# Kernel optimization log

Hardware: AMD Instinct MI355X
Metric: run time of the kernel (lower is better)

## Reference

```python
import jax, jax.numpy as jnp
import numpy as np


def setup_inputs() -> dict:
    key = jax.random.key(0)
    ks = jax.random.split(key, 7)
    S, B, D = 8, 32768, 512
    k = 1.0 / np.sqrt(D)
    u = lambda kk, shape: jax.random.uniform(kk, shape, jnp.float32, -k, k)
    return {
        "x": jax.random.normal(ks[0], (S, B, D), jnp.float32),
        "weight_ih": u(ks[1], (3 * D, D)),
        "weight_hh": u(ks[2], (3 * D, D)),
        "bias_ih": u(ks[3], (3 * D,)),
        "bias_hh": u(ks[4], (3 * D,)),
        "w1": u(ks[5], (D, D)),
        "w2": u(ks[6], (D, D)),
    }


def _gru_cell(xi, h, weight_ih, weight_hh, bias_ih, bias_hh):
    # PyTorch GRUCell gate order: r, z, n
    gi = xi @ weight_ih.T + bias_ih  # [B, 3H]
    gh = h @ weight_hh.T + bias_hh   # [B, 3H]
    i_r, i_z, i_n = jnp.split(gi, 3, axis=-1)
    h_r, h_z, h_n = jnp.split(gh, 3, axis=-1)
    r = jax.nn.sigmoid(i_r + h_r)
    z = jax.nn.sigmoid(i_z + h_z)
    n = jnp.tanh(i_n + r * h_n)
    return (1.0 - z) * n + z * h


def reference(x, weight_ih, weight_hh, bias_ih, bias_hh, w1, w2):
    S, B, _ = x.shape
    H = w1.shape[0]

    def step(carry, inp):
        h, x_prev = carry
        xi, i = inp
        h = _gru_cell(xi, h, weight_ih, weight_hh, bias_ih, bias_hh)
        mixed = h @ w1.T + x_prev @ w2.T  # uses x[i-1]
        h = jnp.where(i % 2 == 1, mixed, h)
        return (h, xi), None

    h0 = jnp.zeros((B, H), x.dtype)  # hn=None -> zeros
    (hn, _), _ = jax.lax.scan(step, (h0, x[0]), (x, jnp.arange(S)))
    return hn
```

## Files before the change

kernel.cpp:

```cpp
#include <hip/hip_runtime.h>


#define BDIM 32768
#define DDIM 512
#define BD (BDIM * DDIM)

typedef short bf16x8 __attribute__((ext_vector_type(8)));
typedef float f32x4 __attribute__((ext_vector_type(4)));
typedef unsigned short u16x8 __attribute__((ext_vector_type(8)));

#define AS1 __attribute__((address_space(1)))
#define AS3 __attribute__((address_space(3)))

__device__ __forceinline__ unsigned short f2bf(float f) {
  union { float f; unsigned u; } v; v.f = f;
  return (unsigned short)((v.u + 0x7fffu + ((v.u >> 16) & 1u)) >> 16);
}
__device__ __forceinline__ float bf2f(unsigned short b) {
  union { unsigned u; float f; } v; v.u = (unsigned)b << 16; return v.f;
}
__device__ __forceinline__ float sigmf(float x) { return 1.0f / (1.0f + __expf(-x)); }
__device__ __forceinline__ float tanhf_(float x) { return 1.0f - 2.0f / (__expf(2.0f * x) + 1.0f); }
__device__ __forceinline__ void bar() { asm volatile("s_barrier" ::: "memory"); }
#define VMCNT(n) asm volatile("s_waitcnt vmcnt(" #n ")" ::: "memory")

__global__ void cvt_bf16_all(const float* __restrict__ in, unsigned short* __restrict__ out) {
  const size_t stride = (size_t)gridDim.x * 256;
  for (size_t i = (size_t)blockIdx.x * 256 + threadIdx.x; i < (size_t)BD; i += stride) {
    const size_t o = i * 8;
    const float4 a = *(const float4*)(in + o);
    const float4 b = *(const float4*)(in + o + 4);
    u16x8 v;
    v[0] = f2bf(a.x); v[1] = f2bf(a.y); v[2] = f2bf(a.z); v[3] = f2bf(a.w);
    v[4] = f2bf(b.x); v[5] = f2bf(b.y); v[6] = f2bf(b.z); v[7] = f2bf(b.w);
    *(u16x8*)(out + o) = v;
  }
}

__global__ void prep_w(const float* __restrict__ wih, const float* __restrict__ whh,
                       const float* __restrict__ w1, const float* __restrict__ w2,
                       unsigned short* __restrict__ Wg, unsigned short* __restrict__ Wm) {
  int i = blockIdx.x * 256 + threadIdx.x;
  if (i < 1536 * 1024) {
    const int j = i >> 10, k = i & 1023;
    Wg[i] = f2bf((k < 512) ? wih[j * 512 + k] : whh[j * 512 + (k - 512)]);
  } else {
    i -= 1536 * 1024;
    const int j = i >> 10, k = i & 1023;
    Wm[i] = f2bf((k < 512) ? w1[j * 512 + k] : w2[j * 512 + (k - 512)]);
  }
}

__global__ __launch_bounds__(512, 2) void gru_gates(
    const unsigned short* __restrict__ X, const unsigned short* __restrict__ H,
    const unsigned short* __restrict__ Wg, const float* __restrict__ bih,
    const float* __restrict__ bhh, unsigned short* __restrict__ outB) {
  __shared__ char smem[147456];
  const int t = threadIdx.x;
  const int lane = t & 63, wid = t >> 6;
  const int wm = wid >> 1, wn = wid & 1;
  const int xcd = blockIdx.x & 7, ixc = blockIdx.x >> 3;
  const int bm = xcd * 16 + (ixc >> 3);
  const int bn = ixc & 7;

  f32x4 acc[4][8];
  const f32x4 z4 = {0.f, 0.f, 0.f, 0.f};
#pragma unroll
  for (int a = 0; a < 4; ++a)
#pragma unroll
    for (int b = 0; b < 8; ++b) acc[a][b] = z4;

  const int trow = t >> 3;
  const int tswz = ((t & 7) * 16) ^ ((trow & 7) << 4);
  int asrc[4], bsrc[3];
#pragma unroll
  for (int i = 0; i < 4; ++i) asrc[i] = (bm * 256 + i * 64 + trow) * 1024 + tswz;
#pragma unroll
  for (int g = 0; g < 3; ++g) bsrc[g] = (g * 512 + bn * 64 + trow) * 2048 + tswz;

  const char* Xc = (const char*)X;
  const char* Hc = (const char*)H;
  const char* Wc = (const char*)Wg;

  auto issA = [&](int tt, int i) {
    const char* base = ((tt < 8) ? Xc : Hc) + (tt & 7) * 128 + asrc[i];
    __builtin_amdgcn_global_load_lds(
        (const AS1 void*)base,
        (AS3 void*)(smem + (tt % 3) * 32768 + i * 8192 + t * 16), 16, 0, 0);
  };
  auto issB = [&](int tt, int g) {
    const char* base = Wc + tt * 128 + bsrc[g];
    __builtin_amdgcn_global_load_lds(
        (const AS1 void*)base,
        (AS3 void*)(smem + 98304 + (tt & 1) * 24576 + g * 8192 + t * 16), 16, 0, 0);
  };

  issB(0, 0); issB(0, 1); issB(0, 2);
  issA(0, 0); issA(0, 1); issA(0, 2); issA(0, 3);
  issA(1, 0); issA(1, 1); issA(1, 2); issA(1, 3);

#pragma unroll
  for (int kt = 0; kt < 16; ++kt) {
    if (kt < 15) { VMCNT(4); } else { VMCNT(0); }
    bar();
    const char* pa = smem + (kt % 3) * 32768;
    const char* pb = smem + 98304 + (kt & 1) * 24576;
    bf16x8 av[4][2], bv[6][2];
#pragma unroll
    for (int ks = 0; ks < 2; ++ks) {
      const int ksb = ks * 64 + (lane >> 4) * 16;
#pragma unroll
      for (int fm = 0; fm < 4; ++fm) {
        const int r = wm * 64 + fm * 16 + (lane & 15);
        av[fm][ks] = *(const bf16x8*)(pa + r * 128 + (ksb ^ ((r & 7) << 4)));
      }
#pragma unroll
      for (int fn = 0; fn < 6; ++fn) {
        const int c = (fn >> 1) * 64 + (fn & 1) * 32 + wn * 16 + (lane & 15);
        bv[fn][ks] = *(const bf16x8*)(pb + c * 128 + (ksb ^ ((c & 7) << 4)));
      }
    }
    if (kt + 1 < 16) { issB(kt + 1, 0); issB(kt + 1, 1); issB(kt + 1, 2); }
    if (kt + 2 < 16) { issA(kt + 2, 0); issA(kt + 2, 1); issA(kt + 2, 2); issA(kt + 2, 3); }
    __builtin_amdgcn_s_setprio(1);
#pragma unroll
    for (int ks = 0; ks < 2; ++ks)
#pragma unroll
      for (int fn = 0; fn < 6; ++fn) {
        const int ai = (fn < 4 || kt < 8) ? fn : fn + 2;
#pragma unroll
        for (int fm = 0; fm < 4; ++fm)
          acc[fm][ai] = __builtin_amdgcn_mfma_f32_16x16x32_bf16(av[fm][ks], bv[fn][ks],
                                                               acc[fm][ai], 0, 0, 0);
      }
    __builtin_amdgcn_s_setprio(0);
    bar();
  }

  const int erow = (lane >> 4) * 4, ecol = lane & 15;
#pragma unroll
  for (int e = 0; e < 2; ++e) {
    const int d = bn * 64 + e * 32 + wn * 16 + ecol;
    const float br = bih[d] + bhh[d];
    const float bz = bih[512 + d] + bhh[512 + d];
    const float bi = bih[1024 + d];
    const float bh = bhh[1024 + d];
#pragma unroll
    for (int fm = 0; fm < 4; ++fm)
#pragma unroll
      for (int j = 0; j < 4; ++j) {
        const int row = bm * 256 + wm * 64 + fm * 16 + erow + j;
        const size_t off = (size_t)row * 512 + d;
        const float rv = sigmf(acc[fm][0 + e][j] + br);
        const float zv = sigmf(acc[fm][2 + e][j] + bz);
        const float nv = tanhf_(acc[fm][4 + e][j] + bi + rv * (acc[fm][6 + e][j] + bh));
        outB[off] = f2bf((1.0f - zv) * nv + zv * bf2f(H[off]));
      }
  }
}

template <int WF>
__global__ __launch_bounds__(512, 2) void mixed_gemm(
    const unsigned short* __restrict__ Ka, const unsigned short* __restrict__ Kb,
    const unsigned short* __restrict__ Wm,
    unsigned short* __restrict__ outB, float* __restrict__ outF) {
  __shared__ char smem[131072];
  const int t = threadIdx.x;
  const int lane = t & 63, wid = t >> 6;
  const int wm = wid >> 1, wn = wid & 1;
  const int xcd = blockIdx.x & 7, ixc = blockIdx.x >> 3;
  const int bm = xcd * 16 + (ixc >> 2);
  const int bn = ixc & 3;

  f32x4 acc[4][4];
  const f32x4 z4 = {0.f, 0.f, 0.f, 0.f};
#pragma unroll
  for (int a = 0; a < 4; ++a)
#pragma unroll
    for (int b = 0; b < 4; ++b) acc[a][b] = z4;

  const int trow = t >> 3;
  const int tswz = ((t & 7) * 16) ^ ((trow & 7) << 4);
  int asrc[4], bsrc[2];
#pragma unroll
  for (int i = 0; i < 4; ++i) asrc[i] = (bm * 256 + i * 64 + trow) * 1024 + tswz;
#pragma unroll
  for (int j = 0; j < 2; ++j) bsrc[j] = (bn * 128 + j * 64 + trow) * 2048 + tswz;

  const char* Kac = (const char*)Ka;
  const char* Kbc = (const char*)Kb;
  const char* Wc = (const char*)Wm;

  auto issA = [&](int tt, int i) {
    const char* base = ((tt < 8) ? Kac : Kbc) + (tt & 7) * 128 + asrc[i];
    __builtin_amdgcn_global_load_lds(
        (const AS1 void*)base,
        (AS3 void*)(smem + (tt % 3) * 32768 + i * 8192 + t * 16), 16, 0, 0);
  };
  auto issB = [&](int tt, int j) {
    const char* base = Wc + tt * 128 + bsrc[j];
    __builtin_amdgcn_global_load_lds(
        (const AS1 void*)base,
        (AS3 void*)(smem + 98304 + (tt & 1) * 16384 + j * 8192 + t * 16), 16, 0, 0);
  };

  issB(0, 0); issB(0, 1);
  issA(0, 0); issA(0, 1); issA(0, 2); issA(0, 3);
  issA(1, 0); issA(1, 1); issA(1, 2); issA(1, 3);

#pragma unroll
  for (int kt = 0; kt < 16; ++kt) {
    if (kt < 15) { VMCNT(4); } else { VMCNT(0); }
    bar();
    const char* pa = smem + (kt % 3) * 32768;
    const char* pb = smem + 98304 + (kt & 1) * 16384;
    bf16x8 av[4][2], bv[4][2];
#pragma unroll
    for (int ks = 0; ks < 2; ++ks) {
      const int ksb = ks * 64 + (lane >> 4) * 16;
#pragma unroll
      for (int fm = 0; fm < 4; ++fm) {
        const int r = wm * 64 + fm * 16 + (lane & 15);
        av[fm][ks] = *(const bf16x8*)(pa + r * 128 + (ksb ^ ((r & 7) << 4)));
      }
#pragma unroll
      for (int fn = 0; fn < 4; ++fn) {
        const int c = wn * 64 + fn * 16 + (lane & 15);
        bv[fn][ks] = *(const bf16x8*)(pb + c * 128 + (ksb ^ ((c & 7) << 4)));
      }
    }
    if (kt + 1 < 16) { issB(kt + 1, 0); issB(kt + 1, 1); }
    if (kt + 2 < 16) { issA(kt + 2, 0); issA(kt + 2, 1); issA(kt + 2, 2); issA(kt + 2, 3); }
    __builtin_amdgcn_s_setprio(1);
#pragma unroll
    for (int ks = 0; ks < 2; ++ks)
#pragma unroll
      for (int fn = 0; fn < 4; ++fn)
#pragma unroll
        for (int fm = 0; fm < 4; ++fm)
          acc[fm][fn] = __builtin_amdgcn_mfma_f32_16x16x32_bf16(av[fm][ks], bv[fn][ks],
                                                               acc[fm][fn], 0, 0, 0);
    __builtin_amdgcn_s_setprio(0);
    bar();
  }

  const int erow = (lane >> 4) * 4, ecol = lane & 15;
#pragma unroll
  for (int fm = 0; fm < 4; ++fm)
#pragma unroll
    for (int fn = 0; fn < 4; ++fn) {
      const int col = bn * 128 + wn * 64 + fn * 16 + ecol;
#pragma unroll
      for (int j = 0; j < 4; ++j) {
        const int row = bm * 256 + wm * 64 + fm * 16 + erow + j;
        const size_t off = (size_t)row * 512 + col;
        const float v = acc[fm][fn][j];
        if constexpr (WF) outF[off] = v;
        else              outB[off] = f2bf(v);
      }
    }
}

extern "C" void kernel_launch(void* const* d_in, const int* in_sizes, int n_in,
                              void* d_out, int out_size, void* d_ws, size_t ws_size,
                              hipStream_t stream) {
  const float* x   = (const float*)d_in[0];
  const float* wih = (const float*)d_in[1];
  const float* whh = (const float*)d_in[2];
  const float* bih = (const float*)d_in[3];
  const float* bhh = (const float*)d_in[4];
  const float* w1  = (const float*)d_in[5];
  const float* w2  = (const float*)d_in[6];

  char* ws = (char*)d_ws;
  const size_t bd2 = (size_t)BD * 2;
  unsigned short* xall  = (unsigned short*)ws;
  unsigned short* hb[2] = {(unsigned short*)(ws + 8 * bd2),
                           (unsigned short*)(ws + 9 * bd2)};
  unsigned short* Wg = (unsigned short*)(ws + 10 * bd2);
  unsigned short* Wm = Wg + 1536 * 1024;

  hipMemsetAsync(hb[0], 0, bd2, stream);
  cvt_bf16_all<<<2048, 256, 0, stream>>>(x, xall);
  prep_w<<<8192, 256, 0, stream>>>(wih, whh, w1, w2, Wg, Wm);

  int hp = 0;
  for (int i = 0; i < 8; ++i) {
    const unsigned short* xi = xall + (size_t)i * BD;
    gru_gates<<<1024, 512, 0, stream>>>(xi, hb[hp], Wg, bih, bhh, hb[hp ^ 1]);
    hp ^= 1;
    if (i & 1) {
      const unsigned short* xprev = xall + (size_t)(i - 1) * BD;
      if (i == 7)
        mixed_gemm<1><<<512, 512, 0, stream>>>(hb[hp], xprev, Wm, nullptr, (float*)d_out);
      else
        mixed_gemm<0><<<512, 512, 0, stream>>>(hb[hp], xprev, Wm, hb[hp ^ 1], nullptr);
      if (i != 7) hp ^= 1;
    }
  }
}
```

Before: 1.280 ms.

## Halve GEMM block tiles to 128 rows with 256 threads and double buffering

```diff
diff --git a/kernel.cpp b/kernel.cpp
--- a/kernel.cpp
+++ b/kernel.cpp
@@ -23,6 +23,8 @@
 __device__ __forceinline__ float tanhf_(float x) { return 1.0f - 2.0f / (__expf(2.0f * x) + 1.0f); }
 __device__ __forceinline__ void bar() { asm volatile("s_barrier" ::: "memory"); }
 #define VMCNT(n) asm volatile("s_waitcnt vmcnt(" #n ")" ::: "memory")
+
+template <int N> struct ICt { static constexpr int v = N; };
 
 __global__ void cvt_bf16_all(const float* __restrict__ in, unsigned short* __restrict__ out) {
   const size_t stride = (size_t)gridDim.x * 256;
@@ -51,16 +53,16 @@
   }
 }
 
-__global__ __launch_bounds__(512, 2) void gru_gates(
+__global__ __launch_bounds__(256, 2) void gru_gates(
     const unsigned short* __restrict__ X, const unsigned short* __restrict__ H,
     const unsigned short* __restrict__ Wg, const float* __restrict__ bih,
     const float* __restrict__ bhh, unsigned short* __restrict__ outB) {
-  __shared__ char smem[147456];
+  __shared__ char smem[81920];
   const int t = threadIdx.x;
   const int lane = t & 63, wid = t >> 6;
   const int wm = wid >> 1, wn = wid & 1;
   const int xcd = blockIdx.x & 7, ixc = blockIdx.x >> 3;
-  const int bm = xcd * 16 + (ixc >> 3);
+  const int bm = xcd * 32 + (ixc >> 3);
   const int bn = ixc & 7;
 
   f32x4 acc[4][8];
@@ -72,75 +74,76 @@
 
   const int trow = t >> 3;
   const int tswz = ((t & 7) * 16) ^ ((trow & 7) << 4);
-  int asrc[4], bsrc[3];
-#pragma unroll
-  for (int i = 0; i < 4; ++i) asrc[i] = (bm * 256 + i * 64 + trow) * 1024 + tswz;
-#pragma unroll
-  for (int g = 0; g < 3; ++g) bsrc[g] = (g * 512 + bn * 64 + trow) * 2048 + tswz;
+  int asrc[4], bsrc[6];
+#pragma unroll
+  for (int i = 0; i < 4; ++i) asrc[i] = (bm * 128 + i * 32 + trow) * 1024 + tswz;
+#pragma unroll
+  for (int j = 0; j < 6; ++j)
+    bsrc[j] = ((j >> 1) * 512 + bn * 64 + (j & 1) * 32 + trow) * 2048 + tswz;
 
   const char* Xc = (const char*)X;
   const char* Hc = (const char*)H;
   const char* Wc = (const char*)Wg;
 
-  auto issA = [&](int tt, int i) {
-    const char* base = ((tt < 8) ? Xc : Hc) + (tt & 7) * 128 + asrc[i];
-    __builtin_amdgcn_global_load_lds(
-        (const AS1 void*)base,
-        (AS3 void*)(smem + (tt % 3) * 32768 + i * 8192 + t * 16), 16, 0, 0);
+  auto stage = [&](int tt) {
+    const char* Ab = ((tt < 8) ? Xc : Hc) + (tt & 7) * 128;
+    const char* Bb = Wc + tt * 128;
+    char* dst = smem + (tt & 1) * 40960;
+#pragma unroll
+    for (int i = 0; i < 4; ++i)
+      __builtin_amdgcn_global_load_lds((const AS1 void*)(Ab + asrc[i]),
+                                       (AS3 void*)(dst + i * 4096 + t * 16), 16, 0, 0);
+#pragma unroll
+    for (int j = 0; j < 6; ++j)
+      __builtin_amdgcn_global_load_lds((const AS1 void*)(Bb + bsrc[j]),
+                                       (AS3 void*)(dst + 16384 + j * 4096 + t * 16), 16, 0, 0);
   };
-  auto issB = [&](int tt, int g) {
-    const char* base = Wc + tt * 128 + bsrc[g];
-    __builtin_amdgcn_global_load_lds(
-        (const AS1 void*)base,
-        (AS3 void*)(smem + 98304 + (tt & 1) * 24576 + g * 8192 + t * 16), 16, 0, 0);
+
+  const int ar0 = wm * 64 + (lane & 15);
+  const int kc0 = (lane >> 4) * 16;
+
+  auto do_tile = [&](int kt, auto nsel) {
+    constexpr int NS = decltype(nsel)::v;
+    VMCNT(0);
+    bar();
+    if (kt + 1 < 16) stage(kt + 1);
+    const char* pa = smem + (kt & 1) * 40960;
+    const char* pb = pa + 16384;
+#pragma unroll
+    for (int ks = 0; ks < 2; ++ks) {
+      bf16x8 av[4], bv[6];
+      const int cb = ks * 64 + kc0;
+#pragma unroll
+      for (int fm = 0; fm < 4; ++fm) {
+        const int r = ar0 + fm * 16;
+        av[fm] = *(const bf16x8*)(pa + r * 128 + (cb ^ ((r & 7) << 4)));
+      }
+#pragma unroll
+      for (int fn = 0; fn < 6; ++fn) {
+        const int r = (fn >> 1) * 64 + wn * 32 + (fn & 1) * 16 + (lane & 15);
+        bv[fn] = *(const bf16x8*)(pb + r * 128 + (cb ^ ((r & 7) << 4)));
+      }
+      __builtin_amdgcn_s_setprio(1);
+#pragma unroll
+      for (int fn = 0; fn < 6; ++fn) {
+        const int ai = (fn < 4) ? fn : NS + (fn - 4);
+#pragma unroll
+        for (int fm = 0; fm < 4; ++fm)
+          acc[fm][ai] = __builtin_amdgcn_mfma_f32_16x16x32_bf16(av[fm], bv[fn],
+                                                               acc[fm][ai], 0, 0, 0);
+      }
+      __builtin_amdgcn_s_setprio(0);
+    }
   };
 
-  issB(0, 0); issB(0, 1); issB(0, 2);
-  issA(0, 0); issA(0, 1); issA(0, 2); issA(0, 3);
-  issA(1, 0); issA(1, 1); issA(1, 2); issA(1, 3);
-
-#pragma unroll
-  for (int kt = 0; kt < 16; ++kt) {
-    if (kt < 15) { VMCNT(4); } else { VMCNT(0); }
-    bar();
-    const char* pa = smem + (kt % 3) * 32768;
-    const char* pb = smem + 98304 + (kt & 1) * 24576;
-    bf16x8 av[4][2], bv[6][2];
-#pragma unroll
-    for (int ks = 0; ks < 2; ++ks) {
-      const int ksb = ks * 64 + (lane >> 4) * 16;
-#pragma unroll
-      for (int fm = 0; fm < 4; ++fm) {
-        const int r = wm * 64 + fm * 16 + (lane & 15);
-        av[fm][ks] = *(const bf16x8*)(pa + r * 128 + (ksb ^ ((r & 7) << 4)));
-      }
-#pragma unroll
-      for (int fn = 0; fn < 6; ++fn) {
-        const int c = (fn >> 1) * 64 + (fn & 1) * 32 + wn * 16 + (lane & 15);
-        bv[fn][ks] = *(const bf16x8*)(pb + c * 128 + (ksb ^ ((c & 7) << 4)));
-      }
-    }
-    if (kt + 1 < 16) { issB(kt + 1, 0); issB(kt + 1, 1); issB(kt + 1, 2); }
-    if (kt + 2 < 16) { issA(kt + 2, 0); issA(kt + 2, 1); issA(kt + 2, 2); issA(kt + 2, 3); }
-    __builtin_amdgcn_s_setprio(1);
-#pragma unroll
-    for (int ks = 0; ks < 2; ++ks)
-#pragma unroll
-      for (int fn = 0; fn < 6; ++fn) {
-        const int ai = (fn < 4 || kt < 8) ? fn : fn + 2;
-#pragma unroll
-        for (int fm = 0; fm < 4; ++fm)
-          acc[fm][ai] = __builtin_amdgcn_mfma_f32_16x16x32_bf16(av[fm][ks], bv[fn][ks],
-                                                               acc[fm][ai], 0, 0, 0);
-      }
-    __builtin_amdgcn_s_setprio(0);
-    bar();
-  }
+  stage(0);
+  for (int kt = 0; kt < 8; ++kt) do_tile(kt, ICt<4>{});
+  for (int kt = 8; kt < 16; ++kt) do_tile(kt, ICt<6>{});
 
   const int erow = (lane >> 4) * 4, ecol = lane & 15;
 #pragma unroll
   for (int e = 0; e < 2; ++e) {
-    const int d = bn * 64 + e * 32 + wn * 16 + ecol;
+    const int d = bn * 64 + wn * 32 + e * 16 + ecol;
     const float br = bih[d] + bhh[d];
     const float bz = bih[512 + d] + bhh[512 + d];
     const float bi = bih[1024 + d];
@@ -149,7 +152,7 @@
     for (int fm = 0; fm < 4; ++fm)
 #pragma unroll
       for (int j = 0; j < 4; ++j) {
-        const int row = bm * 256 + wm * 64 + fm * 16 + erow + j;
+        const int row = bm * 128 + wm * 64 + fm * 16 + erow + j;
         const size_t off = (size_t)row * 512 + d;
         const float rv = sigmf(acc[fm][0 + e][j] + br);
         const float zv = sigmf(acc[fm][2 + e][j] + bz);
@@ -160,16 +163,16 @@
 }
 
 template <int WF>
-__global__ __launch_bounds__(512, 2) void mixed_gemm(
+__global__ __launch_bounds__(256, 2) void mixed_gemm(
     const unsigned short* __restrict__ Ka, const unsigned short* __restrict__ Kb,
     const unsigned short* __restrict__ Wm,
     unsigned short* __restrict__ outB, float* __restrict__ outF) {
-  __shared__ char smem[131072];
+  __shared__ char smem[65536];
   const int t = threadIdx.x;
   const int lane = t & 63, wid = t >> 6;
   const int wm = wid >> 1, wn = wid & 1;
   const int xcd = blockIdx.x & 7, ixc = blockIdx.x >> 3;
-  const int bm = xcd * 16 + (ixc >> 2);
+  const int bm = xcd * 32 + (ixc >> 2);
   const int bn = ixc & 3;
 
   f32x4 acc[4][4];
@@ -181,67 +184,64 @@
 
   const int trow = t >> 3;
   const int tswz = ((t & 7) * 16) ^ ((trow & 7) << 4);
-  int asrc[4], bsrc[2];
-#pragma unroll
-  for (int i = 0; i < 4; ++i) asrc[i] = (bm * 256 + i * 64 + trow) * 1024 + tswz;
-#pragma unroll
-  for (int j = 0; j < 2; ++j) bsrc[j] = (bn * 128 + j * 64 + trow) * 2048 + tswz;
-
+  int asrc[4], bsrc[4];
+#pragma unroll
+  for (int i = 0; i < 4; ++i) {
+    asrc[i] = (bm * 128 + i * 32 + trow) * 1024 + tswz;
+    bsrc[i] = (bn * 128 + i * 32 + trow) * 2048 + tswz;
+  }
   const char* Kac = (const char*)Ka;
   const char* Kbc = (const char*)Kb;
   const char* Wc = (const char*)Wm;
 
-  auto issA = [&](int tt, int i) {
-    const char* base = ((tt < 8) ? Kac : Kbc) + (tt & 7) * 128 + asrc[i];
-    __builtin_amdgcn_global_load_lds(
-        (const AS1 void*)base,
-        (AS3 void*)(smem + (tt % 3) * 32768 + i * 8192 + t * 16), 16, 0, 0);
+  auto stage = [&](int tt) {
+    const char* Ab = ((tt < 8) ? Kac : Kbc) + (tt & 7) * 128;
+    const char* Bb = Wc + tt * 128;
+    char* dst = smem + (tt & 1) * 32768;
+#pragma unroll
+    for (int i = 0; i < 4; ++i)
+      __builtin_amdgcn_global_load_lds((const AS1 void*)(Ab + asrc[i]),
+                                       (AS3 void*)(dst + i * 4096 + t * 16), 16, 0, 0);
+#pragma unroll
+    for (int j = 0; j < 4; ++j)
+      __builtin_amdgcn_global_load_lds((const AS1 void*)(Bb + bsrc[j]),
+                                       (AS3 void*)(dst + 16384 + j * 4096 + t * 16), 16, 0, 0);
   };
-  auto issB = [&](int tt, int j) {
-    const char* base = Wc + tt * 128 + bsrc[j];
-    __builtin_amdgcn_global_load_lds(
-        (const AS1 void*)base,
-        (AS3 void*)(smem + 98304 + (tt & 1) * 16384 + j * 8192 + t * 16), 16, 0, 0);
-  };
-
-  issB(0, 0); issB(0, 1);
-  issA(0, 0); issA(0, 1); issA(0, 2); issA(0, 3);
-  issA(1, 0); issA(1, 1); issA(1, 2); issA(1, 3);
-
-#pragma unroll
+
+  const int ar0 = wm * 64 + (lane & 15);
+  const int br0 = wn * 64 + (lane & 15);
+  const int kc0 = (lane >> 4) * 16;
+
+  stage(0);
   for (int kt = 0; kt < 16; ++kt) {
-    if (kt < 15) { VMCNT(4); } else { VMCNT(0); }
+    VMCNT(0);
     bar();
-    const char* pa = smem + (kt % 3) * 32768;
-    const char* pb = smem + 98304 + (kt & 1) * 16384;
-    bf16x8 av[4][2], bv[4][2];
+    if (kt + 1 < 16) stage(kt + 1);
+    const char* pa = smem + (kt & 1) * 32768;
+    const char* pb = pa + 16384;
 #pragma unroll
     for (int ks = 0; ks < 2; ++ks) {
-      const int ksb = ks * 64 + (lane >> 4) * 16;
+      bf16x8 av[4], bv[4];
+      const int cb = ks * 64 + kc0;
 #pragma unroll
       for (int fm = 0; fm < 4; ++fm) {
-        const int r = wm * 64 + fm * 16 + (lane & 15);
-        av[fm][ks] = *(const bf16x8*)(pa + r * 128 + (ksb ^ ((r & 7) << 4)));
+        const int r = ar0 + fm * 16;
+        av[fm] = *(const bf16x8*)(pa + r * 128 + (cb ^ ((r & 7) << 4)));
       }
 #pragma unroll
       for (int fn = 0; fn < 4; ++fn) {
-        const int c = wn * 64 + fn * 16 + (lane & 15);
-        bv[fn][ks] = *(const bf16x8*)(pb + c * 128 + (ksb ^ ((c & 7) << 4)));
-      }
+        const int r = br0 + fn * 16;
+        bv[fn] = *(const bf16x8*)(pb + r * 128 + (cb ^ ((r & 7) << 4)));
+      }
+      __builtin_amdgcn_s_setprio(1);
+#pragma unroll
+      for (int fn = 0; fn < 4; ++fn)
+#pragma unroll
+        for (int fm = 0; fm < 4; ++fm)
+          acc[fm][fn] = __builtin_amdgcn_mfma_f32_16x16x32_bf16(av[fm], bv[fn],
+                                                               acc[fm][fn], 0, 0, 0);
+      __builtin_amdgcn_s_setprio(0);
     }
-    if (kt + 1 < 16) { issB(kt + 1, 0); issB(kt + 1, 1); }
-    if (kt + 2 < 16) { issA(kt + 2, 0); issA(kt + 2, 1); issA(kt + 2, 2); issA(kt + 2, 3); }
-    __builtin_amdgcn_s_setprio(1);
-#pragma unroll
-    for (int ks = 0; ks < 2; ++ks)
-#pragma unroll
-      for (int fn = 0; fn < 4; ++fn)
-#pragma unroll
-        for (int fm = 0; fm < 4; ++fm)
-          acc[fm][fn] = __builtin_amdgcn_mfma_f32_16x16x32_bf16(av[fm][ks], bv[fn][ks],
-                                                               acc[fm][fn], 0, 0, 0);
-    __builtin_amdgcn_s_setprio(0);
-    bar();
   }
 
   const int erow = (lane >> 4) * 4, ecol = lane & 15;
@@ -252,7 +252,7 @@
       const int col = bn * 128 + wn * 64 + fn * 16 + ecol;
 #pragma unroll
       for (int j = 0; j < 4; ++j) {
-        const int row = bm * 256 + wm * 64 + fm * 16 + erow + j;
+        const int row = bm * 128 + wm * 64 + fm * 16 + erow + j;
         const size_t off = (size_t)row * 512 + col;
         const float v = acc[fm][fn][j];
         if constexpr (WF) outF[off] = v;
@@ -287,14 +287,14 @@
   int hp = 0;
   for (int i = 0; i < 8; ++i) {
     const unsigned short* xi = xall + (size_t)i * BD;
-    gru_gates<<<1024, 512, 0, stream>>>(xi, hb[hp], Wg, bih, bhh, hb[hp ^ 1]);
+    gru_gates<<<2048, 256, 0, stream>>>(xi, hb[hp], Wg, bih, bhh, hb[hp ^ 1]);
     hp ^= 1;
     if (i & 1) {
       const unsigned short* xprev = xall + (size_t)(i - 1) * BD;
       if (i == 7)
-        mixed_gemm<1><<<512, 512, 0, stream>>>(hb[hp], xprev, Wm, nullptr, (float*)d_out);
+        mixed_gemm<1><<<1024, 256, 0, stream>>>(hb[hp], xprev, Wm, nullptr, (float*)d_out);
       else
-        mixed_gemm<0><<<512, 512, 0, stream>>>(hb[hp], xprev, Wm, hb[hp ^ 1], nullptr);
+        mixed_gemm<0><<<1024, 256, 0, stream>>>(hb[hp], xprev, Wm, hb[hp ^ 1], nullptr);
       if (i != 7) hp ^= 1;
     }
   }
```

Result: faster. 1.194 ms (-6.7%).
